# Kernel optimization log

Hardware: AMD Instinct MI355X
Metric: run time of the kernel (lower is better)

The kernel has to match this reference:

```python
import jax, jax.numpy as jnp
import numpy as np

B, T, DIM = 4, 2048, 1024
H, DH = 16, 64  # num_heads, dim_head; weight_dim = H*DH = 1024
SCALE = DIM ** (-0.5)  # note: original scales by dim**-0.5, not dim_head**-0.5


def setup_inputs() -> dict:
    key = jax.random.key(0)
    k1, k2, k3 = jax.random.split(key, 3)
    x = jax.random.normal(k1, (B, T, DIM), dtype=jnp.float32)
    w_qkv = jax.random.normal(k2, (3 * H * DH, DIM), dtype=jnp.float32) * (DIM ** -0.5)
    w_out = jax.random.normal(k3, (DIM, H * DH), dtype=jnp.float32) * ((H * DH) ** -0.5)
    b_out = jnp.zeros((DIM,), dtype=jnp.float32)
    return {"x": x, "w_qkv": w_qkv, "w_out": w_out, "b_out": b_out}


def reference(x, w_qkv, w_out, b_out):
    # qkv: [b, t, 3*H*DH] (torch Linear: x @ W^T)
    qkv = jnp.einsum('btc,oc->bto', x, w_qkv)
    # rearrange 'b t (d k h) -> k b h t d' with k=3, h=H: d is the OUTERMOST
    # factor of the flattened axis, then k, then h (h fastest-varying).
    qkv = qkv.reshape(B, T, DH, 3, H)          # [b, t, d, k, h]
    qkv = jnp.transpose(qkv, (3, 0, 4, 1, 2))   # [k, b, h, t, d]
    q, k, v = qkv[0], qkv[1], qkv[2]
    # scores: [b, h, t, t]
    attn = jnp.einsum('bhid,bhjd->bhij', q, k) * SCALE
    attn = jax.nn.softmax(attn, axis=-1)
    out = jnp.einsum('bhij,bhjd->bhid', attn, v)           # [b, h, t, d]
    out = jnp.transpose(out, (0, 2, 1, 3)).reshape(B, T, H * DH)  # 'b h t d -> b t (h d)'
    return jnp.einsum('btc,oc->bto', out, w_out) + b_out
```

## Files before the change

kernel.cpp:

```cpp
#include <hip/hip_runtime.h>
#include <hip/hip_bf16.h>


typedef __attribute__((ext_vector_type(8))) short short8;
typedef __attribute__((ext_vector_type(4))) float floatx4;

static __device__ __forceinline__ floatx4 mfma16(short8 a, short8 b, floatx4 c) {
    return __builtin_amdgcn_mfma_f32_16x16x32_bf16(a, b, c, 0, 0, 0);
}

static __device__ __forceinline__ unsigned short f2bf_bits(float f) {
    __hip_bfloat16 h = __float2bfloat16(f);
    return *reinterpret_cast<unsigned short*>(&h);
}

static __device__ __forceinline__ float fast_exp2(float x) {
#if __has_builtin(__builtin_amdgcn_exp2f)
    return __builtin_amdgcn_exp2f(x);
#else
    return exp2f(x);
#endif
}

__global__ __launch_bounds__(256) void k_cvt(
    const float* __restrict__ src, unsigned short* __restrict__ dst, int n4)
{
    typedef __attribute__((ext_vector_type(4))) unsigned short ushort4v;
    for (int i = blockIdx.x * blockDim.x + threadIdx.x; i < n4;
         i += gridDim.x * blockDim.x) {
        const float4 v = ((const float4*)src)[i];
        ushort4v o;
        o.x = f2bf_bits(v.x);
        o.y = f2bf_bits(v.y);
        o.z = f2bf_bits(v.z);
        o.w = f2bf_bits(v.w);
        ((ushort4v*)dst)[i] = o;
    }
}

__global__ __launch_bounds__(256) void k_qkv(
    const unsigned short* __restrict__ x,
    const unsigned short* __restrict__ w,
    unsigned short* __restrict__ qb,
    unsigned short* __restrict__ kb,
    unsigned short* __restrict__ vb)
{
    __shared__ unsigned short As[128 * 40];
    __shared__ unsigned short Bs[128 * 40];

    const int tid  = threadIdx.x;
    const int wave = tid >> 6, lane = tid & 63;
    const int quad = lane >> 4, l16 = lane & 15;
    const int wm = wave >> 1, wn = wave & 1;
    const int m0 = blockIdx.y * 128;
    const int kk = blockIdx.x >> 3;
    const int d0 = (blockIdx.x & 7) * 8;
    const int kkh = kk * 16;

    floatx4 acc[4][4];
#pragma unroll
    for (int i = 0; i < 4; i++)
#pragma unroll
        for (int j = 0; j < 4; j++) acc[i][j] = (floatx4){0.f, 0.f, 0.f, 0.f};

    const int srow = tid >> 2;
    const int scc  = (tid & 3) * 8;

    for (int k0 = 0; k0 < 1024; k0 += 32) {
#pragma unroll
        for (int i = 0; i < 2; i++) {
            const int row = srow + i * 64;
            const int bn  = (d0 + (row >> 4)) * 48 + kkh + (row & 15);
            *(uint4*)&As[row * 40 + scc] = *(const uint4*)&x[(m0 + row) * 1024 + k0 + scc];
            *(uint4*)&Bs[row * 40 + scc] = *(const uint4*)&w[bn * 1024 + k0 + scc];
        }
        __syncthreads();

        short8 af[4], bfv[4];
#pragma unroll
        for (int mi = 0; mi < 4; mi++)
            af[mi] = *(const short8*)&As[(wm * 64 + mi * 16 + l16) * 40 + quad * 8];
#pragma unroll
        for (int ni = 0; ni < 4; ni++)
            bfv[ni] = *(const short8*)&Bs[(wn * 64 + ni * 16 + l16) * 40 + quad * 8];
#pragma unroll
        for (int mi = 0; mi < 4; mi++)
#pragma unroll
            for (int ni = 0; ni < 4; ni++)
                acc[mi][ni] = mfma16(af[mi], bfv[ni], acc[mi][ni]);
        __syncthreads();
    }

    unsigned short* dst = (kk == 0) ? qb : (kk == 1) ? kb : vb;
    const float scale = (kk == 0) ? 0.045084220027780106f : 1.0f;
#pragma unroll
    for (int ni = 0; ni < 4; ni++) {
        const int d = d0 + wn * 4 + ni;
#pragma unroll
        for (int mi = 0; mi < 4; mi++) {
            const int m  = m0 + wm * 64 + mi * 16 + quad * 4;
            const int b  = m >> 11;
            const int tt = m & 2047;
            ushort4 pk;
            pk.x = f2bf_bits(acc[mi][ni][0] * scale);
            pk.y = f2bf_bits(acc[mi][ni][1] * scale);
            pk.z = f2bf_bits(acc[mi][ni][2] * scale);
            pk.w = f2bf_bits(acc[mi][ni][3] * scale);
            *(ushort4*)&dst[((b * 16 + l16) * 64 + d) * 2048 + tt] = pk;
        }
    }
}

__global__ __launch_bounds__(256) void k_tr(
    const unsigned short* __restrict__ src,
    unsigned short* __restrict__ dst)
{
    __shared__ unsigned short Ts[64 * 72];
    const int tid = threadIdx.x;
    const int bh  = blockIdx.y;
    const int t0  = blockIdx.x * 64;
    const int dg  = (tid >> 4) * 4;
    const int tg  = (tid & 15) * 4;

    ushort4 rv[4];
#pragma unroll
    for (int dd = 0; dd < 4; dd++)
        rv[dd] = *(const ushort4*)&src[(bh * 64 + dg + dd) * 2048 + t0 + tg];
#pragma unroll
    for (int tt = 0; tt < 4; tt++) {
        ushort4 wv;
        wv.x = ((const unsigned short*)&rv[0])[tt];
        wv.y = ((const unsigned short*)&rv[1])[tt];
        wv.z = ((const unsigned short*)&rv[2])[tt];
        wv.w = ((const unsigned short*)&rv[3])[tt];
        *(ushort4*)&Ts[(tg + tt) * 72 + dg] = wv;
    }
    __syncthreads();

    const int tr = tid >> 2;
    const int c8 = (tid & 3) * 8;
    *(uint4*)&dst[(bh * 2048 + t0 + tr) * 64 + c8]      = *(const uint4*)&Ts[tr * 72 + c8];
    *(uint4*)&dst[(bh * 2048 + t0 + tr) * 64 + c8 + 32] = *(const uint4*)&Ts[tr * 72 + c8 + 32];
}

__global__ __launch_bounds__(512) void k_attn(
    const unsigned short* __restrict__ qt,
    const unsigned short* __restrict__ kt,
    const unsigned short* __restrict__ vg,
    __hip_bfloat16* __restrict__ og)
{
    __shared__ unsigned short Ks[64 * 72];
    __shared__ unsigned short Vt[64 * 72];
    __shared__ unsigned short Pt[8 * 32 * 72];

    const int tid  = threadIdx.x;
    const int wave = tid >> 6, lane = tid & 63;
    const int quad = lane >> 4, l16 = lane & 15;
    const int blk = blockIdx.x;
    const int bh  = (blk & 7) | ((blk >> 6) << 3);
    const int q0  = ((blk >> 3) & 7) * 256;
    const int qr  = q0 + wave * 32;

    short8 qf[2][2];
#pragma unroll
    for (int mi = 0; mi < 2; mi++)
#pragma unroll
        for (int ks = 0; ks < 2; ks++)
            qf[mi][ks] = *(const short8*)&qt[(bh * 2048 + qr + mi * 16 + l16) * 64 + ks * 32 + quad * 8];

    float lsum[2][4];
    floatx4 o[2][4];
#pragma unroll
    for (int mi = 0; mi < 2; mi++)
#pragma unroll
        for (int r = 0; r < 4; r++) lsum[mi][r] = 0.f;
#pragma unroll
    for (int mi = 0; mi < 2; mi++)
#pragma unroll
        for (int di = 0; di < 4; di++) o[mi][di] = (floatx4){0.f, 0.f, 0.f, 0.f};

    const int srow = tid >> 3;
    const int sc8  = (tid & 7) * 8;

    for (int j0 = 0; j0 < 2048; j0 += 64) {
        *(uint4*)&Ks[srow * 72 + sc8] = *(const uint4*)&kt[(bh * 2048 + j0 + srow) * 64 + sc8];
        *(uint4*)&Vt[srow * 72 + sc8] = *(const uint4*)&vg[(bh * 64 + srow) * 2048 + j0 + sc8];
        __syncthreads();

        floatx4 s[2][4];
#pragma unroll
        for (int mi = 0; mi < 2; mi++)
#pragma unroll
            for (int ni = 0; ni < 4; ni++) s[mi][ni] = (floatx4){0.f, 0.f, 0.f, 0.f};
#pragma unroll
        for (int ks = 0; ks < 2; ks++) {
            short8 kf[4];
#pragma unroll
            for (int ni = 0; ni < 4; ni++)
                kf[ni] = *(const short8*)&Ks[(ni * 16 + l16) * 72 + ks * 32 + quad * 8];
#pragma unroll
            for (int mi = 0; mi < 2; mi++)
#pragma unroll
                for (int ni = 0; ni < 4; ni++)
                    s[mi][ni] = mfma16(qf[mi][ks], kf[ni], s[mi][ni]);
        }

#pragma unroll
        for (int mi = 0; mi < 2; mi++)
#pragma unroll
            for (int ni = 0; ni < 4; ni++)
#pragma unroll
                for (int r = 0; r < 4; r++) {
                    const float p = fast_exp2(s[mi][ni][r]);
                    lsum[mi][r] += p;
                    ((__hip_bfloat16*)Pt)[(wave * 32 + mi * 16 + quad * 4 + r) * 72 + ni * 16 + l16] =
                        __float2bfloat16(p);
                }
        __builtin_amdgcn_s_waitcnt(0xc07f);

#pragma unroll
        for (int ks = 0; ks < 2; ks++) {
            short8 pf[2], vf[4];
#pragma unroll
            for (int mi = 0; mi < 2; mi++)
                pf[mi] = *(const short8*)&Pt[(wave * 32 + mi * 16 + l16) * 72 + ks * 32 + quad * 8];
#pragma unroll
            for (int di = 0; di < 4; di++)
                vf[di] = *(const short8*)&Vt[(di * 16 + l16) * 72 + ks * 32 + quad * 8];
#pragma unroll
            for (int mi = 0; mi < 2; mi++)
#pragma unroll
                for (int di = 0; di < 4; di++)
                    o[mi][di] = mfma16(pf[mi], vf[di], o[mi][di]);
        }
        __syncthreads();
    }

    const int b = bh >> 4, h = bh & 15;
#pragma unroll
    for (int mi = 0; mi < 2; mi++) {
#pragma unroll
        for (int r = 0; r < 4; r++) {
            float rs = lsum[mi][r];
            rs += __shfl_xor(rs, 1);
            rs += __shfl_xor(rs, 2);
            rs += __shfl_xor(rs, 4);
            rs += __shfl_xor(rs, 8);
            const float inv = 1.0f / rs;
            const int t = qr + mi * 16 + quad * 4 + r;
#pragma unroll
            for (int di = 0; di < 4; di++)
                og[(b * 2048 + t) * 1024 + h * 64 + di * 16 + l16] =
                    __float2bfloat16(o[mi][di][r] * inv);
        }
    }
}

__global__ __launch_bounds__(256) void k_out(
    const unsigned short* __restrict__ a,
    const unsigned short* __restrict__ w,
    const float* __restrict__ bias,
    float* __restrict__ out)
{
    __shared__ unsigned short As[128 * 40];
    __shared__ unsigned short Bs[128 * 40];

    const int tid  = threadIdx.x;
    const int wave = tid >> 6, lane = tid & 63;
    const int quad = lane >> 4, l16 = lane & 15;
    const int wm = wave >> 1, wn = wave & 1;
    const int m0 = blockIdx.y * 128, n0 = blockIdx.x * 128;

    floatx4 acc[4][4];
#pragma unroll
    for (int i = 0; i < 4; i++)
#pragma unroll
        for (int j = 0; j < 4; j++) acc[i][j] = (floatx4){0.f, 0.f, 0.f, 0.f};

    const int srow = tid >> 2;
    const int scc  = (tid & 3) * 8;

    for (int k0 = 0; k0 < 1024; k0 += 32) {
#pragma unroll
        for (int i = 0; i < 2; i++) {
            const int row = srow + i * 64;
            *(uint4*)&As[row * 40 + scc] = *(const uint4*)&a[(m0 + row) * 1024 + k0 + scc];
            *(uint4*)&Bs[row * 40 + scc] = *(const uint4*)&w[(n0 + row) * 1024 + k0 + scc];
        }
        __syncthreads();

        short8 af[4], bfv[4];
#pragma unroll
        for (int mi = 0; mi < 4; mi++)
            af[mi] = *(const short8*)&As[(wm * 64 + mi * 16 + l16) * 40 + quad * 8];
#pragma unroll
        for (int ni = 0; ni < 4; ni++)
            bfv[ni] = *(const short8*)&Bs[(wn * 64 + ni * 16 + l16) * 40 + quad * 8];
#pragma unroll
        for (int mi = 0; mi < 4; mi++)
#pragma unroll
            for (int ni = 0; ni < 4; ni++)
                acc[mi][ni] = mfma16(af[mi], bfv[ni], acc[mi][ni]);
        __syncthreads();
    }

#pragma unroll
    for (int ni = 0; ni < 4; ni++) {
        const int col = n0 + wn * 64 + ni * 16 + l16;
        const float bv = bias[col];
#pragma unroll
        for (int mi = 0; mi < 4; mi++) {
            const int mbase = m0 + wm * 64 + mi * 16 + quad * 4;
#pragma unroll
            for (int r = 0; r < 4; r++)
                out[(mbase + r) * 1024 + col] = acc[mi][ni][r] + bv;
        }
    }
}

extern "C" void kernel_launch(void* const* d_in, const int* in_sizes, int n_in,
                              void* d_out, int out_size, void* d_ws, size_t ws_size,
                              hipStream_t stream) {
    const float* x    = (const float*)d_in[0];
    const float* wqkv = (const float*)d_in[1];
    const float* wout = (const float*)d_in[2];
    const float* bout = (const float*)d_in[3];
    float* out = (float*)d_out;

    unsigned short* ws = (unsigned short*)d_ws;
    unsigned short* xb    = ws;
    unsigned short* wqkvb = xb + 8388608;
    unsigned short* woutb = wqkvb + 3145728;
    unsigned short* qb    = woutb + 1048576;
    unsigned short* kb    = qb + 8388608;
    unsigned short* vb    = kb + 8388608;
    unsigned short* ob    = vb + 8388608;

    k_cvt<<<2048, 256, 0, stream>>>(x,    xb,    8388608 / 4);
    k_cvt<<<1024, 256, 0, stream>>>(wqkv, wqkvb, 3145728 / 4);
    k_cvt<<<512,  256, 0, stream>>>(wout, woutb, 1048576 / 4);

    k_qkv<<<dim3(24, 64), 256, 0, stream>>>(xb, wqkvb, qb, kb, vb);

    k_tr<<<dim3(32, 64), 256, 0, stream>>>(qb, xb);
    k_tr<<<dim3(32, 64), 256, 0, stream>>>(kb, qb);

    k_attn<<<512, 512, 0, stream>>>(xb, qb, vb, (__hip_bfloat16*)ob);
    k_out<<<dim3(8, 64), 256, 0, stream>>>(ob, woutb, bout, out);
}
```

Before: 312.2 us.

## Use direct global-to-LDS loads in GEMMs and transpose score MFMA in attention

The QKV and output projection GEMMs now stage tiles through global_load_lds (16-byte direct-to-LDS loads) instead of loading into registers and then storing to LDS. The padded row stride is dropped so each wave fills contiguous 16-row chunks. In attention, the QK^T MFMA operands are swapped so each lane holds four consecutive keys for one query row. This allows packed 8-byte P stores and a per-lane row-sum that needs only two cross-lane shuffles. Risks are more LDS bank conflicts from the unpadded stride, and no explicit wait on the async LDS loads beyond the barrier.

```diff
diff --git a/kernel.cpp b/kernel.cpp
--- a/kernel.cpp
+++ b/kernel.cpp
@@ -21,6 +21,11 @@
     return exp2f(x);
 #endif
 }
+
+#define GLD16(gptr, ldsptr)                                                  \
+    __builtin_amdgcn_global_load_lds(                                        \
+        (const __attribute__((address_space(1))) void*)(gptr),               \
+        (__attribute__((address_space(3))) void*)(ldsptr), 16, 0, 0)
 
 __global__ __launch_bounds__(256) void k_cvt(
     const float* __restrict__ src, unsigned short* __restrict__ dst, int n4)
@@ -40,13 +45,13 @@
 
 __global__ __launch_bounds__(256) void k_qkv(
     const unsigned short* __restrict__ x,
-    const unsigned short* __restrict__ w,
+    const unsigned short* __restrict__ wq,
     unsigned short* __restrict__ qb,
     unsigned short* __restrict__ kb,
     unsigned short* __restrict__ vb)
 {
-    __shared__ unsigned short As[128 * 40];
-    __shared__ unsigned short Bs[128 * 40];
+    __shared__ unsigned short As[128 * 32];
+    __shared__ unsigned short Bs[128 * 32];
 
     const int tid  = threadIdx.x;
     const int wave = tid >> 6, lane = tid & 63;
@@ -57,32 +62,33 @@
     const int d0 = (blockIdx.x & 7) * 8;
     const int kkh = kk * 16;
 
+    const int srow = lane >> 2;
+    const int sc8  = (lane & 3) * 8;
+    const int row0 = wave * 32 + srow;
+    const int row1 = row0 + 16;
+    const int bn0  = (d0 + (row0 >> 4)) * 48 + kkh + (row0 & 15);
+    const int bn1  = (d0 + (row1 >> 4)) * 48 + kkh + (row1 & 15);
+
     floatx4 acc[4][4];
 #pragma unroll
     for (int i = 0; i < 4; i++)
 #pragma unroll
         for (int j = 0; j < 4; j++) acc[i][j] = (floatx4){0.f, 0.f, 0.f, 0.f};
 
-    const int srow = tid >> 2;
-    const int scc  = (tid & 3) * 8;
-
     for (int k0 = 0; k0 < 1024; k0 += 32) {
-#pragma unroll
-        for (int i = 0; i < 2; i++) {
-            const int row = srow + i * 64;
-            const int bn  = (d0 + (row >> 4)) * 48 + kkh + (row & 15);
-            *(uint4*)&As[row * 40 + scc] = *(const uint4*)&x[(m0 + row) * 1024 + k0 + scc];
-            *(uint4*)&Bs[row * 40 + scc] = *(const uint4*)&w[bn * 1024 + k0 + scc];
-        }
+        GLD16(&x[(m0 + row0) * 1024 + k0 + sc8], &As[(wave * 32) * 32]);
+        GLD16(&x[(m0 + row1) * 1024 + k0 + sc8], &As[(wave * 32 + 16) * 32]);
+        GLD16(&wq[bn0 * 1024 + k0 + sc8],        &Bs[(wave * 32) * 32]);
+        GLD16(&wq[bn1 * 1024 + k0 + sc8],        &Bs[(wave * 32 + 16) * 32]);
         __syncthreads();
 
         short8 af[4], bfv[4];
 #pragma unroll
         for (int mi = 0; mi < 4; mi++)
-            af[mi] = *(const short8*)&As[(wm * 64 + mi * 16 + l16) * 40 + quad * 8];
+            af[mi] = *(const short8*)&As[(wm * 64 + mi * 16 + l16) * 32 + quad * 8];
 #pragma unroll
         for (int ni = 0; ni < 4; ni++)
-            bfv[ni] = *(const short8*)&Bs[(wn * 64 + ni * 16 + l16) * 40 + quad * 8];
+            bfv[ni] = *(const short8*)&Bs[(wn * 64 + ni * 16 + l16) * 32 + quad * 8];
 #pragma unroll
         for (int mi = 0; mi < 4; mi++)
 #pragma unroll
@@ -168,12 +174,8 @@
         for (int ks = 0; ks < 2; ks++)
             qf[mi][ks] = *(const short8*)&qt[(bh * 2048 + qr + mi * 16 + l16) * 64 + ks * 32 + quad * 8];
 
-    float lsum[2][4];
+    float lsum[2] = {0.f, 0.f};
     floatx4 o[2][4];
-#pragma unroll
-    for (int mi = 0; mi < 2; mi++)
-#pragma unroll
-        for (int r = 0; r < 4; r++) lsum[mi][r] = 0.f;
 #pragma unroll
     for (int mi = 0; mi < 2; mi++)
 #pragma unroll
@@ -187,35 +189,41 @@
         *(uint4*)&Vt[srow * 72 + sc8] = *(const uint4*)&vg[(bh * 64 + srow) * 2048 + j0 + sc8];
         __syncthreads();
 
-        floatx4 s[2][4];
+        floatx4 st[2][4];
 #pragma unroll
         for (int mi = 0; mi < 2; mi++)
 #pragma unroll
-            for (int ni = 0; ni < 4; ni++) s[mi][ni] = (floatx4){0.f, 0.f, 0.f, 0.f};
+            for (int nk = 0; nk < 4; nk++) st[mi][nk] = (floatx4){0.f, 0.f, 0.f, 0.f};
 #pragma unroll
         for (int ks = 0; ks < 2; ks++) {
             short8 kf[4];
 #pragma unroll
-            for (int ni = 0; ni < 4; ni++)
-                kf[ni] = *(const short8*)&Ks[(ni * 16 + l16) * 72 + ks * 32 + quad * 8];
+            for (int nk = 0; nk < 4; nk++)
+                kf[nk] = *(const short8*)&Ks[(nk * 16 + l16) * 72 + ks * 32 + quad * 8];
 #pragma unroll
             for (int mi = 0; mi < 2; mi++)
 #pragma unroll
-                for (int ni = 0; ni < 4; ni++)
-                    s[mi][ni] = mfma16(qf[mi][ks], kf[ni], s[mi][ni]);
-        }
-
-#pragma unroll
-        for (int mi = 0; mi < 2; mi++)
-#pragma unroll
-            for (int ni = 0; ni < 4; ni++)
-#pragma unroll
-                for (int r = 0; r < 4; r++) {
-                    const float p = fast_exp2(s[mi][ni][r]);
-                    lsum[mi][r] += p;
-                    ((__hip_bfloat16*)Pt)[(wave * 32 + mi * 16 + quad * 4 + r) * 72 + ni * 16 + l16] =
-                        __float2bfloat16(p);
-                }
+                for (int nk = 0; nk < 4; nk++)
+                    st[mi][nk] = mfma16(kf[nk], qf[mi][ks], st[mi][nk]);
+        }
+
+#pragma unroll
+        for (int mi = 0; mi < 2; mi++) {
+#pragma unroll
+            for (int nk = 0; nk < 4; nk++) {
+                const float p0 = fast_exp2(st[mi][nk][0]);
+                const float p1 = fast_exp2(st[mi][nk][1]);
+                const float p2 = fast_exp2(st[mi][nk][2]);
+                const float p3 = fast_exp2(st[mi][nk][3]);
+                lsum[mi] += (p0 + p1) + (p2 + p3);
+                ushort4 pk;
+                pk.x = f2bf_bits(p0);
+                pk.y = f2bf_bits(p1);
+                pk.z = f2bf_bits(p2);
+                pk.w = f2bf_bits(p3);
+                *(ushort4*)&Pt[(wave * 32 + mi * 16 + l16) * 72 + nk * 16 + quad * 4] = pk;
+            }
+        }
         __builtin_amdgcn_s_waitcnt(0xc07f);
 
 #pragma unroll
@@ -236,17 +244,20 @@
         __syncthreads();
     }
 
+#pragma unroll
+    for (int mi = 0; mi < 2; mi++) {
+        float t = lsum[mi];
+        t += __shfl_xor(t, 16);
+        t += __shfl_xor(t, 32);
+        lsum[mi] = t;
+    }
+
     const int b = bh >> 4, h = bh & 15;
 #pragma unroll
     for (int mi = 0; mi < 2; mi++) {
 #pragma unroll
         for (int r = 0; r < 4; r++) {
-            float rs = lsum[mi][r];
-            rs += __shfl_xor(rs, 1);
-            rs += __shfl_xor(rs, 2);
-            rs += __shfl_xor(rs, 4);
-            rs += __shfl_xor(rs, 8);
-            const float inv = 1.0f / rs;
+            const float inv = 1.0f / __shfl(lsum[mi], quad * 4 + r);
             const int t = qr + mi * 16 + quad * 4 + r;
 #pragma unroll
             for (int di = 0; di < 4; di++)
@@ -258,12 +269,12 @@
 
 __global__ __launch_bounds__(256) void k_out(
     const unsigned short* __restrict__ a,
-    const unsigned short* __restrict__ w,
+    const unsigned short* __restrict__ wq,
     const float* __restrict__ bias,
     float* __restrict__ out)
 {
-    __shared__ unsigned short As[128 * 40];
-    __shared__ unsigned short Bs[128 * 40];
+    __shared__ unsigned short As[128 * 32];
+    __shared__ unsigned short Bs[128 * 32];
 
     const int tid  = threadIdx.x;
     const int wave = tid >> 6, lane = tid & 63;
@@ -271,31 +282,31 @@
     const int wm = wave >> 1, wn = wave & 1;
     const int m0 = blockIdx.y * 128, n0 = blockIdx.x * 128;
 
+    const int srow = lane >> 2;
+    const int sc8  = (lane & 3) * 8;
+    const int row0 = wave * 32 + srow;
+    const int row1 = row0 + 16;
+
     floatx4 acc[4][4];
 #pragma unroll
     for (int i = 0; i < 4; i++)
 #pragma unroll
         for (int j = 0; j < 4; j++) acc[i][j] = (floatx4){0.f, 0.f, 0.f, 0.f};
 
-    const int srow = tid >> 2;
-    const int scc  = (tid & 3) * 8;
-
     for (int k0 = 0; k0 < 1024; k0 += 32) {
-#pragma unroll
-        for (int i = 0; i < 2; i++) {
-            const int row = srow + i * 64;
-            *(uint4*)&As[row * 40 + scc] = *(const uint4*)&a[(m0 + row) * 1024 + k0 + scc];
-            *(uint4*)&Bs[row * 40 + scc] = *(const uint4*)&w[(n0 + row) * 1024 + k0 + scc];
-        }
+        GLD16(&a[(m0 + row0) * 1024 + k0 + sc8],  &As[(wave * 32) * 32]);
+        GLD16(&a[(m0 + row1) * 1024 + k0 + sc8],  &As[(wave * 32 + 16) * 32]);
+        GLD16(&wq[(n0 + row0) * 1024 + k0 + sc8], &Bs[(wave * 32) * 32]);
+        GLD16(&wq[(n0 + row1) * 1024 + k0 + sc8], &Bs[(wave * 32 + 16) * 32]);
         __syncthreads();
 
         short8 af[4], bfv[4];
 #pragma unroll
         for (int mi = 0; mi < 4; mi++)
-            af[mi] = *(const short8*)&As[(wm * 64 + mi * 16 + l16) * 40 + quad * 8];
+            af[mi] = *(const short8*)&As[(wm * 64 + mi * 16 + l16) * 32 + quad * 8];
 #pragma unroll
         for (int ni = 0; ni < 4; ni++)
-            bfv[ni] = *(const short8*)&Bs[(wn * 64 + ni * 16 + l16) * 40 + quad * 8];
+            bfv[ni] = *(const short8*)&Bs[(wn * 64 + ni * 16 + l16) * 32 + quad * 8];
 #pragma unroll
         for (int mi = 0; mi < 4; mi++)
 #pragma unroll
```

Measured after the change: 308.4 us. Within noise of the previous version (-1.2%).
